# Kernel tuning notes

Hardware: AMD Instinct MI355X
Metric: run time of the kernel (lower is better)

## Reference

```python
import jax, jax.numpy as jnp
import numpy as np

B, H, W = 8, 128, 128
WIDTH, MODES = 32, 12
NL = 6


def _spectral_conv(x, w):
    # x: [B,C,H,W] real; w: [2, Cin, Cout, m, m, 2] (real/imag packed)
    b, c, h, ww = x.shape
    m = w.shape[3]
    xf = jnp.fft.rfft2(x)  # [B,C,H,W//2+1] complex
    w1 = w[0, ..., 0] + 1j * w[0, ..., 1]
    w2 = w[1, ..., 0] + 1j * w[1, ..., 1]
    top = jnp.einsum('bixy,ioxy->boxy', xf[:, :, :m, :m], w1)
    bot = jnp.einsum('bixy,ioxy->boxy', xf[:, :, -m:, :m], w2)
    out = jnp.zeros((b, w.shape[2], h, ww // 2 + 1), dtype=xf.dtype)
    out = out.at[:, :, :m, :m].set(top).at[:, :, -m:, :m].set(bot)
    return jnp.fft.irfft2(out, s=(h, ww))


def _conv1x1(x, wgt, bia):
    # x: [B,C,H,W], wgt: [O,C], bia: [O]
    return jnp.einsum('bchw,oc->bohw', x, wgt) + bia[None, :, None, None]


def _gelu(x):
    return jax.nn.gelu(x, approximate=False)


def setup_inputs() -> dict:
    key = jax.random.key(0)
    ks = jax.random.split(key, 20)
    scale = 1.0 / (WIDTH * WIDTH)
    d = {}
    d['x'] = jax.random.normal(ks[0], (B, H, W, 4), jnp.float32)
    d['fc0_W'] = jax.random.normal(ks[1], (4, WIDTH), jnp.float32) * 0.5
    d['fc0_b'] = jnp.zeros((WIDTH,), jnp.float32)
    d['spec_w'] = scale * jax.random.uniform(ks[2], (NL, 2, WIDTH, WIDTH, MODES, MODES, 2), jnp.float32)
    d['wW'] = jax.random.normal(ks[3], (NL, WIDTH, WIDTH), jnp.float32) * (1.0 / np.sqrt(WIDTH))
    d['wb'] = jnp.zeros((NL, WIDTH), jnp.float32)
    d['bW'] = jax.random.normal(ks[4], (NL, WIDTH, 2), jnp.float32) * 0.7
    d['bb'] = jnp.zeros((NL, WIDTH), jnp.float32)
    d['cW'] = jax.random.normal(ks[5], (NL, WIDTH, 3), jnp.float32) * 0.57
    d['cb'] = jnp.zeros((NL, WIDTH), jnp.float32)
    d['fc1_W'] = jax.random.normal(ks[6], (WIDTH, 256), jnp.float32) * (1.0 / np.sqrt(WIDTH))
    d['fc1_b'] = jnp.zeros((256,), jnp.float32)
    d['fc3_W'] = jax.random.normal(ks[7], (256, 128), jnp.float32) * (1.0 / 16.0)
    d['fc3_b'] = jnp.zeros((128,), jnp.float32)
    d['fc4_W'] = jax.random.normal(ks[8], (128, 128), jnp.float32) * (1.0 / np.sqrt(128.0))
    d['fc4_b'] = jnp.zeros((128,), jnp.float32)
    d['fc5_W'] = jax.random.normal(ks[9], (128, 1), jnp.float32) * (1.0 / np.sqrt(128.0))
    d['fc5_b'] = jnp.zeros((1,), jnp.float32)
    return d


def reference(x, fc0_W, fc0_b, spec_w, wW, wb, bW, bb, cW, cb,
              fc1_W, fc1_b, fc3_W, fc3_b, fc4_W, fc4_b, fc5_W, fc5_b):
    b, h, w, _ = x.shape
    grid_mesh = jnp.transpose(x[:, :, :, 1:4], (0, 3, 1, 2))  # [B,3,H,W]
    y = x @ fc0_W + fc0_b                                     # [B,H,W,width]
    y = jnp.transpose(y, (0, 3, 1, 2))                        # [B,width,H,W]
    gx = jnp.linspace(0.0, 1.0, h, dtype=jnp.float32)
    gy = jnp.linspace(0.0, 1.0, w, dtype=jnp.float32)
    grid = jnp.stack([
        jnp.broadcast_to(gx[:, None], (h, w)),
        jnp.broadcast_to(gy[None, :], (h, w)),
    ], axis=0)                                                # [2,H,W]
    grid = jnp.broadcast_to(grid[None], (b, 2, h, w))
    for l in range(NL):
        y = _gelu(_spectral_conv(y, spec_w[l])
                  + _conv1x1(y, wW[l], wb[l])
                  + _conv1x1(grid, bW[l], bb[l])
                  + _conv1x1(grid_mesh, cW[l], cb[l]))
    y = jnp.transpose(y, (0, 2, 3, 1))                        # [B,H,W,width]
    y = _gelu(y @ fc1_W + fc1_b)
    y = _gelu(y @ fc3_W + fc3_b)
    y = y @ fc4_W + fc4_b
    y = y @ fc5_W + fc5_b
    return y
```

## Files before the change

### kernel.cpp

```cpp
#include <hip/hip_runtime.h>
#include <math.h>


#define NL 6

typedef unsigned short u16;
typedef __attribute__((ext_vector_type(8))) short short8v;
typedef __attribute__((ext_vector_type(8))) unsigned short ushort8v;
typedef __attribute__((ext_vector_type(4))) unsigned short ushort4v;
typedef __attribute__((ext_vector_type(4))) float f32x4;

__device__ __forceinline__ float gelu_f(float x){
  float z  = x*0.70710678118654752f;
  float az = fabsf(z);
  float t  = __builtin_amdgcn_rcpf(fmaf(0.3275911f, az, 1.0f));
  float p  = t*(0.254829592f + t*(-0.284496736f + t*(1.421413741f +
             t*(-1.453152027f + t*1.061405429f))));
  float e  = __expf(-z*z);
  float er = copysignf(fmaf(-p, e, 1.0f), z);
  return 0.5f*x*(1.0f + er);
}
__device__ __forceinline__ u16 f2bf(float x){
  unsigned u = __float_as_uint(x);
  u += 0x7FFF + ((u>>16)&1);
  return (u16)(u>>16);
}
__device__ __forceinline__ float bf2f(u16 h){
  return __uint_as_float(((unsigned)h)<<16);
}
__device__ __forceinline__ void split2(float v, u16 &hh, u16 &ll){
  unsigned u = __float_as_uint(v);
  hh = (u16)(u>>16);
  float lo = v - __uint_as_float(u & 0xFFFF0000u);
  ll = (u16)(__float_as_uint(lo)>>16);
}

__global__ __launch_bounds__(256) void k_fc0f(const float* __restrict__ x,
                      const float* __restrict__ W, const float* __restrict__ b,
                      float* __restrict__ y, float* __restrict__ F1){
  __shared__ float Ws[128];
  __shared__ float bs[32];
  __shared__ float ys2[2][32][132];
  int t = threadIdx.x;
  if (t < 128) Ws[t] = W[t];
  if (t < 32)  bs[t] = b[t];
  __syncthreads();
  int pix = blockIdx.x*256 + t;
  float4 xv = *reinterpret_cast<const float4*>(x + (size_t)pix*4);
  int bb = pix >> 14, hw = pix & 16383;
  int r = t>>7, w = t&127;
  float* yp = y + (size_t)bb*32*16384 + hw;
  #pragma unroll
  for (int c=0;c<32;c++){
    float acc = bs[c] + xv.x*Ws[c] + xv.y*Ws[32+c] + xv.z*Ws[64+c] + xv.w*Ws[96+c];
    yp[(size_t)c*16384] = acc;
    ys2[r][c][w] = acc;
  }
  __syncthreads();
  int c2 = t>>3, wq = t&7;
  float stc[12], sts[12];
  #pragma unroll
  for (int k=0;k<12;k++){ float s,c; sincospif(k*(1.0f/64.0f), &s, &c); stc[k]=c; sts[k]=s; }
  int gr0 = blockIdx.x*2;
  #pragma unroll
  for (int r2=0;r2<2;r2++){
    float cr[12], ci[12], aR[12], aI[12];
    #pragma unroll
    for (int k=0;k<12;k++){
      float s,c; sincospif((float)(k*wq)*0.25f, &s, &c);
      cr[k]=c; ci[k]=s; aR[k]=0.f; aI[k]=0.f;
    }
    const float* rowp = &ys2[r2][c2][wq*16];
    #pragma unroll
    for (int q=0;q<4;q++){
      float4 xq = *reinterpret_cast<const float4*>(rowp + q*4);
      float xa[4]={xq.x,xq.y,xq.z,xq.w};
      #pragma unroll
      for (int e=0;e<4;e++){
        float xw = xa[e];
        #pragma unroll
        for (int k=0;k<12;k++){
          aR[k] += xw*cr[k];
          aI[k] -= xw*ci[k];
          float nc = cr[k]*stc[k] - ci[k]*sts[k];
          ci[k]    = cr[k]*sts[k] + ci[k]*stc[k];
          cr[k] = nc;
        }
      }
    }
    #pragma unroll
    for (int k=0;k<12;k++){
      aR[k] += __shfl_xor(aR[k],1); aR[k] += __shfl_xor(aR[k],2); aR[k] += __shfl_xor(aR[k],4);
      aI[k] += __shfl_xor(aI[k],1); aI[k] += __shfl_xor(aI[k],2); aI[k] += __shfl_xor(aI[k],4);
    }
    if (wq==0){
      int g = gr0 + r2; int b2 = g>>7, h2 = g&127;
      float* dst = F1 + ((size_t)(b2*32+c2)*128 + h2)*24;
      #pragma unroll
      for (int k=0;k<12;k++){ dst[2*k] = aR[k]; dst[2*k+1] = aI[k]; }
    }
  }
}

__global__ __launch_bounds__(256) void k_wtrans(const float* __restrict__ w, float* __restrict__ wT){
  __shared__ float buf[16][32][25];
  int t=threadIdx.x;
  int beta = blockIdx.x;
  int l = beta/48, r = beta%48;
  int hf = r/24; int r2 = r%24;
  int kym = r2>>1; int i0 = (r2&1)*16;
  const float* src = w + (size_t)l*589824 + (size_t)hf*294912 + kym*24;
  float* dst = wT + (size_t)l*589824 + (size_t)hf*294912 + (size_t)kym*24576;
  for (int j=t; j<12288; j+=256){
    int i = j/768, rem = j%768, o = rem/24, kxri = rem%24;
    buf[i][o][kxri] = src[(size_t)(i0+i)*9216 + o*288 + kxri];
  }
  __syncthreads();
  for (int j=t; j<12288; j+=256){
    int kx = j>>10, rem = j&1023, i = rem>>6, orr = rem&63, o = orr>>1, ri = orr&1;
    dst[(size_t)kx*2048 + o*64 + (i0+i)*2 + ri] = buf[i][o][kx*2+ri];
  }
}

__global__ __launch_bounds__(256) void k_wprep(const float* __restrict__ W1, const float* __restrict__ W3,
                       const float* __restrict__ W4,
                       const float* __restrict__ b4, const float* __restrict__ w5,
                       const float* __restrict__ b5,
                       u16* __restrict__ W1h, u16* __restrict__ W1l,
                       u16* __restrict__ W3h, u16* __restrict__ W3l,
                       u16* __restrict__ W4h, u16* __restrict__ W4l,
                       u16* __restrict__ Emh, u16* __restrict__ Eml,
                       u16* __restrict__ E2h, u16* __restrict__ E2l,
                       u16* __restrict__ E3h, u16* __restrict__ E3l,
                       float* __restrict__ c45){
  __shared__ float buf[32][132];
  int t = threadIdx.x, bid = blockIdx.x;
  if (bid < 8){
    int k0 = bid*32;
    for (int i=t;i<4096;i+=256){ int k=i>>7, n=i&127; buf[k][n] = W3[(size_t)(k0+k)*128 + n]; }
    __syncthreads();
    int n = t>>1, kq = t&1;
    #pragma unroll
    for (int kk=0;kk<16;kk++){
      int k = kq*16 + kk;
      float v = buf[k][n];
      u16 hh = f2bf(v);
      W3h[(size_t)bid*4096 + n*32 + k] = hh;
      W3l[(size_t)bid*4096 + n*32 + k] = f2bf(v - bf2f(hh));
    }
  } else if (bid == 8){
    __shared__ float red[256];
    int n = t;
    #pragma unroll
    for (int c=0;c<32;c++){
      float v = W1[(size_t)c*256 + n];
      u16 hh = f2bf(v);
      W1h[n*32 + c] = hh;
      W1l[n*32 + c] = f2bf(v - bf2f(hh));
    }
    red[t] = (t<128)? b4[t]*w5[t] : 0.f;
    __syncthreads();
    for (int s2=128; s2>0; s2>>=1){
      if (t<s2) red[t] += red[t+s2];
      __syncthreads();
    }
    if (t==0) c45[0] = red[0] + b5[0];
  } else if (bid <= 12){
    int k0 = (bid-9)*32;
    for (int i=t;i<4096;i+=256){ int k=i>>7, n=i&127; buf[k][n] = W4[(size_t)(k0+k)*128 + n]; }
    __syncthreads();
    int n = t>>1, kq = t&1;
    #pragma unroll
    for (int kk=0;kk<16;kk++){
      int k = kq*16 + kk;
      float v = buf[k][n];
      u16 hh = f2bf(v);
      W4h[(size_t)(bid-9)*4096 + n*32 + k] = hh;
      W4l[(size_t)(bid-9)*4096 + n*32 + k] = f2bf(v - bf2f(hh));
    }
  } else if (bid == 13){
    for (int i=t;i<4096;i+=256){
      int m=i>>7, w=i&127;
      float v=0.f;
      if (m<24){ float s,c; sincospif((float)((m>>1)*w)*(1.0f/64.0f), &s, &c); v = (m&1)? -s : c; }
      u16 hh, ll; split2(v, hh, ll);
      Emh[i]=hh; Eml[i]=ll;
    }
  } else if (bid == 14){
    for (int i=t;i<12288;i+=256){
      int m=i>>8, k=i&255;
      int kyi = (m<24)? m : m-24;
      int ky  = (kyi<12)? kyi : kyi+104;
      int h   = k&127;
      int mm  = (ky*h)&127;
      float s,c; sincospif((float)mm*(1.0f/64.0f), &s, &c);
      bool sinSlot = k>=128;
      float v;
      if (m<24) v = sinSlot? s : c;
      else      v = sinSlot? c : -s;
      u16 hh, ll; split2(v, hh, ll);
      E2h[i]=hh; E2l[i]=ll;
    }
  } else {
    for (int i=t;i<8192;i+=256){
      int h=i>>6, k=i&63;
      float v=0.f;
      if (k<48){
        int kyi = (k<24)? k : k-24;
        int ky  = (kyi<12)? kyi : kyi+104;
        int mm  = (ky*h)&127;
        float s,c; sincospif((float)mm*(1.0f/64.0f), &s, &c);
        v = ((k<24)? c : s) * (1.0f/16384.0f);
      }
      u16 hh, ll; split2(v, hh, ll);
      E3h[i]=hh; E3l[i]=ll;
    }
  }
}

__global__ __launch_bounds__(256) void k_dfth(const float* __restrict__ F1,
                      const u16* __restrict__ E2h, const u16* __restrict__ E2l,
                      float* __restrict__ F2){
  __shared__ u16 Fth[16*264], Ftl[16*264];
  int t=threadIdx.x;
  int bc = blockIdx.x;
  int b = bc>>5, c = bc&31;
  const float* src = F1 + (size_t)bc*3072;
  for (int i=t;i<3072;i+=256){
    int h = i/24, col = i - h*24;
    int kx = col>>1, ri = col&1;
    u16 hh, ll; split2(src[i], hh, ll);
    int idx = kx*264 + ri*128 + h;
    Fth[idx] = hh; Ftl[idx] = ll;
  }
  __syncthreads();
  int wv = t>>6, lane = t&63, lr = lane&15, lg = lane>>4;
  if (wv < 3){
    f32x4 acc = (f32x4){0.f,0.f,0.f,0.f};
    #pragma unroll
    for (int ks=0; ks<8; ++ks){
      short8v af = *reinterpret_cast<const short8v*>(E2h + (size_t)(wv*16+lr)*256 + ks*32 + lg*8);
      short8v ag = *reinterpret_cast<const short8v*>(E2l + (size_t)(wv*16+lr)*256 + ks*32 + lg*8);
      short8v bf = *reinterpret_cast<const short8v*>(&Fth[lr*264 + ks*32 + lg*8]);
      short8v bg = *reinterpret_cast<const short8v*>(&Ftl[lr*264 + ks*32 + lg*8]);
      acc = __builtin_amdgcn_mfma_f32_16x16x32_bf16(af, bf, acc, 0,0,0);
      acc = __builtin_amdgcn_mfma_f32_16x16x32_bf16(af, bg, acc, 0,0,0);
      acc = __builtin_amdgcn_mfma_f32_16x16x32_bf16(ag, bf, acc, 0,0,0);
    }
    if (lr < 12){
      #pragma unroll
      for (int r=0;r<4;r++){
        int m = wv*16 + 4*lg + r;
        int kyi = (m<24)? m : m-24;
        int ri  = (m<24)? 0 : 1;
        F2[(((size_t)b*24 + kyi)*24 + 2*lr + ri)*32 + c] = acc[r];
      }
    }
  }
}

__global__ __launch_bounds__(576) void k_mixid(const float* __restrict__ F2, const float* __restrict__ wTl,
                      const u16* __restrict__ E3h, const u16* __restrict__ E3l,
                      float* __restrict__ S1){
  __shared__ u16 Bh[32*72], Bl[32*72];
  int t=threadIdx.x;
  int bo = blockIdx.x;
  int b = bo>>5, o = bo&31;
  for (int i=t; i<24*24; i+=576){
    int row = i/24, k = 48 + i - (i/24)*24;
    Bh[row*72 + k] = 0; Bl[row*72 + k] = 0;
  }
  {
    int pair = t>>1, half = t&1;
    int kx = pair%12, kyi = pair/12;
    int hf = kyi<12?0:1, kym = kyi<12?kyi:kyi-12;
    const float* fpr = F2 + (((size_t)b*24 + kyi)*24 + 2*kx)*32 + half*16;
    const float* fpi = fpr + 32;
    const float* wp = wTl + (size_t)(hf*12+kym)*24576 + kx*2048 + o*64 + half*32;
    float gr=0.f, gi=0.f;
    #pragma unroll 8
    for (int i=0;i<16;i++){
      float2 wv = *reinterpret_cast<const float2*>(wp + 2*i);
      float ar = fpr[i], ai = fpi[i];
      gr += ar*wv.x - ai*wv.y;
      gi += ar*wv.y + ai*wv.x;
    }
    gr += __shfl_xor(gr,1);
    gi += __shfl_xor(gi,1);
    if (half==0){
      u16 grh, grl, gih, gil, nih, nil;
      split2(gr, grh, grl);
      split2(gi, gih, gil);
      split2(-gi, nih, nil);
      int r0 = (2*kx)*72, r1 = (2*kx+1)*72;
      Bh[r0 + kyi]      = grh; Bl[r0 + kyi]      = grl;
      Bh[r0 + 24 + kyi] = nih; Bl[r0 + 24 + kyi] = nil;
      Bh[r1 + kyi]      = gih; Bl[r1 + kyi]      = gil;
      Bh[r1 + 24 + kyi] = grh; Bl[r1 + 24 + kyi] = grl;
    }
  }
  __syncthreads();
  int wv = t>>6, lane = t&63, lr = lane&15, lg = lane>>4;
  if (wv < 8){
    f32x4 acc[2];
    acc[0] = (f32x4){0.f,0.f,0.f,0.f};
    acc[1] = (f32x4){0.f,0.f,0.f,0.f};
    #pragma unroll
    for (int ks=0; ks<2; ++ks){
      short8v af = *reinterpret_cast<const short8v*>(E3h + (size_t)(wv*16+lr)*64 + ks*32 + lg*8);
      short8v ag = *reinterpret_cast<const short8v*>(E3l + (size_t)(wv*16+lr)*64 + ks*32 + lg*8);
      #pragma unroll
      for (int nt=0; nt<2; ++nt){
        short8v bf = *reinterpret_cast<const short8v*>(&Bh[(nt*16+lr)*72 + ks*32 + lg*8]);
        short8v bg = *reinterpret_cast<const short8v*>(&Bl[(nt*16+lr)*72 + ks*32 + lg*8]);
        acc[nt] = __builtin_amdgcn_mfma_f32_16x16x32_bf16(af, bf, acc[nt], 0,0,0);
        acc[nt] = __builtin_amdgcn_mfma_f32_16x16x32_bf16(af, bg, acc[nt], 0,0,0);
        acc[nt] = __builtin_amdgcn_mfma_f32_16x16x32_bf16(ag, bf, acc[nt], 0,0,0);
      }
    }
    float* dst = S1 + (size_t)bo*3072;
    #pragma unroll
    for (int nt=0; nt<2; ++nt){
      int n = nt*16 + lr;
      if (n < 24){
        #pragma unroll
        for (int r=0;r<4;r++){
          int h = wv*16 + 4*lg + r;
          dst[h*24 + n] = acc[nt][r];
        }
      }
    }
  }
}

template<int LAST>
__global__ __launch_bounds__(512) void k_combine2(const float* __restrict__ yin, const float* __restrict__ S1,
                         const float* __restrict__ x,
                         const float* __restrict__ wWl, const float* __restrict__ wbl,
                         const float* __restrict__ bWl, const float* __restrict__ bbl,
                         const float* __restrict__ cWl, const float* __restrict__ cbl,
                         const u16* __restrict__ Emh, const u16* __restrict__ Eml,
                         float* __restrict__ yout, float* __restrict__ F1,
                         u16* __restrict__ yb16){
  __shared__ float ysT[128][33];
  __shared__ u16 ybsp[2][32][136];
  int t=threadIdx.x;
  int b = blockIdx.x>>7, h = blockIdx.x&127;
  for (int i=t;i<4096;i+=512){ int c=i>>7, w=i&127;
    ysT[w][c] = yin[(((size_t)(b*32+c))*128+h)*128+w]; }
  __syncthreads();
  int w = t&127;
  int og = __builtin_amdgcn_readfirstlane(t>>7);
  float ct[12], st[12];
  ct[0]=1.f; st[0]=0.f;
  float c1,s1v; sincospif(w*(1.0f/64.0f), &s1v, &c1);
  #pragma unroll
  for (int k=0;k<11;k++){ ct[k+1] = ct[k]*c1 - st[k]*s1v; st[k+1] = ct[k]*s1v + st[k]*c1; }
  float gx = h*(1.0f/127.0f), gy = w*(1.0f/127.0f);
  float4 xm = *reinterpret_cast<const float4*>(x + (((size_t)(b*128+h))*128+w)*4);
  float m1=xm.y, m2=xm.z, m3=xm.w;
  const float* wo  = wWl + og*256;
  const float* s1o = S1 + (size_t)b*98304 + (size_t)og*8*3072 + h*24;
  float accv[8];
  #pragma unroll
  for (int oi=0;oi<8;oi++){
    int o = og*8+oi;
    float bse = wbl[o] + bbl[o] + cbl[o] + gx*bWl[o*2] + gy*bWl[o*2+1]
              + m1*cWl[o*3] + m2*cWl[o*3+1] + m3*cWl[o*3+2];
    const float* sp = s1o + (size_t)oi*3072;
    float spec = sp[0];
    #pragma unroll
    for (int kx=1;kx<12;kx++) spec += 2.0f*(sp[2*kx]*ct[kx] - sp[2*kx+1]*st[kx]);
    accv[oi] = bse + spec;
  }
  #pragma unroll
  for (int c=0;c<32;c++){
    float xc = ysT[w][c];
    #pragma unroll
    for (int oi=0;oi<8;oi++) accv[oi] += wo[oi*32+c]*xc;
  }
  #pragma unroll
  for (int oi=0;oi<8;oi++){
    float g = gelu_f(accv[oi]);
    int o = og*8+oi;
    if constexpr (!LAST){
      u16 hh, ll; split2(g, hh, ll);
      ybsp[0][o][w] = hh;
      ybsp[1][o][w] = ll;
      yout[(((size_t)(b*32+o))*128+h)*128+w] = g;
    } else {
      ybsp[0][o][w] = f2bf(g);
    }
  }
  __syncthreads();
  if constexpr (!LAST){
    int wv = t>>6;
    if (wv < 4){
      int lane = t&63, lr = lane&15, lg = lane>>4;
      int mt = wv&1, oj = wv>>1;
      f32x4 acc = (f32x4){0.f,0.f,0.f,0.f};
      #pragma unroll
      for (int ks=0; ks<4; ++ks){
        short8v ef = *reinterpret_cast<const short8v*>(Emh + (size_t)(mt*16+lr)*128 + ks*32 + lg*8);
        short8v eg = *reinterpret_cast<const short8v*>(Eml + (size_t)(mt*16+lr)*128 + ks*32 + lg*8);
        short8v yf = *reinterpret_cast<const short8v*>(&ybsp[0][oj*16+lr][ks*32+lg*8]);
        short8v yg = *reinterpret_cast<const short8v*>(&ybsp[1][oj*16+lr][ks*32+lg*8]);
        acc = __builtin_amdgcn_mfma_f32_16x16x32_bf16(ef, yf, acc, 0,0,0);
        acc = __builtin_amdgcn_mfma_f32_16x16x32_bf16(ef, yg, acc, 0,0,0);
        acc = __builtin_amdgcn_mfma_f32_16x16x32_bf16(eg, yf, acc, 0,0,0);
      }
      if (mt==0 || lg<2){
        int m = mt*16 + 4*lg;
        int o = oj*16 + lr;
        float4 v; v.x=acc[0]; v.y=acc[1]; v.z=acc[2]; v.w=acc[3];
        *reinterpret_cast<float4*>(&F1[((size_t)(b*32+o)*128 + h)*24 + m]) = v;
      }
    }
  } else {
    int wr = t>>2, hf4 = t&3;
    size_t pix = (size_t)b*16384 + h*128 + wr;
    ushort8v h8;
    #pragma unroll
    for (int q=0;q<8;q++) h8[q] = ybsp[0][hf4*8 + q][wr];
    *reinterpret_cast<ushort8v*>(yb16 + pix*32 + hf4*8) = h8;
  }
}

__global__ __launch_bounds__(256) void k_headm(
    const u16* __restrict__ Yb,
    const u16* __restrict__ W1h, const u16* __restrict__ W1l,
    const float* __restrict__ b1,
    const u16* __restrict__ W3h, const u16* __restrict__ W3l,
    const float* __restrict__ b3,
    const u16* __restrict__ W4h, const u16* __restrict__ W4l,
    const float* __restrict__ c45, const float* __restrict__ w5,
    float* __restrict__ out){
  __shared__ u16 smem[8704];
  __shared__ float b1s[256];
  __shared__ float b3s[128], w5s[128];
  __shared__ float part2[2][64];
  int t = threadIdx.x;
  int wv = t>>6, lane = t&63, lr = lane&15, lg = lane>>4;
  int P0 = blockIdx.x*64;
  b1s[t] = b1[t];
  if (t<128){ b3s[t]=b3[t]; w5s[t]=w5[t]; }
  int wn3 = wv>>1, wp = wv&1;
  short8v yb;
  {
    size_t p = (size_t)P0 + wv*16 + lr;
    yb = *reinterpret_cast<const short8v*>(Yb + p*32 + lg*8);
  }
  f32x4 acc3[4][2];
  #pragma unroll
  for (int i=0;i<4;i++){ acc3[i][0]=(f32x4){0,0,0,0}; acc3[i][1]=(f32x4){0,0,0,0}; }
  __syncthreads();

  auto fc1_into = [&](int kt, u16* dh){
    f32x4 a1[2];
    a1[0]=(f32x4){0,0,0,0}; a1[1]=(f32x4){0,0,0,0};
    #pragma unroll
    for (int i=0;i<2;i++){
      int n1 = kt*32 + i*16 + lr;
      short8v w1f = *reinterpret_cast<const short8v*>(W1h + (size_t)n1*32 + lg*8);
      short8v w1g = *reinterpret_cast<const short8v*>(W1l + (size_t)n1*32 + lg*8);
      a1[i] = __builtin_amdgcn_mfma_f32_16x16x32_bf16(w1f, yb, a1[i], 0,0,0);
      a1[i] = __builtin_amdgcn_mfma_f32_16x16x32_bf16(w1g, yb, a1[i], 0,0,0);
    }
    #pragma unroll
    for (int i=0;i<2;i++){
      int n1b = kt*32 + i*16 + 4*lg;
      int p = wv*16 + lr;
      ushort4v hv;
      #pragma unroll
      for (int r=0;r<4;r++){
        hv[r] = f2bf(gelu_f(a1[i][r] + b1s[n1b+r]));
      }
      *reinterpret_cast<ushort4v*>(&dh[p*40 + i*16+4*lg]) = hv;
    }
  };

  fc1_into(0, smem);
  __syncthreads();
  for (int kt=0; kt<8; ++kt){
    u16* curh = (kt&1)? smem + 2560 : smem;
    if (kt < 7){
      u16* nh = (kt&1)? smem : smem + 2560;
      fc1_into(kt+1, nh);
    }
    short8v ab[2];
    #pragma unroll
    for (int j=0;j<2;j++){
      int pb = wp*32 + j*16 + lr;
      ab[j] = *reinterpret_cast<const short8v*>(&curh[pb*40 + lg*8]);
    }
    #pragma unroll
    for (int i=0;i<4;i++){
      int n3 = wn3*64 + i*16 + lr;
      short8v w3f = *reinterpret_cast<const short8v*>(W3h + (size_t)kt*4096 + n3*32 + lg*8);
      short8v w3g = *reinterpret_cast<const short8v*>(W3l + (size_t)kt*4096 + n3*32 + lg*8);
      #pragma unroll
      for (int j=0;j<2;j++){
        acc3[i][j] = __builtin_amdgcn_mfma_f32_16x16x32_bf16(w3f, ab[j], acc3[i][j], 0,0,0);
        acc3[i][j] = __builtin_amdgcn_mfma_f32_16x16x32_bf16(w3g, ab[j], acc3[i][j], 0,0,0);
      }
    }
    __syncthreads();
  }
  u16* A2 = smem;
  #pragma unroll
  for (int i=0;i<4;i++){
    int n3b = wn3*64 + i*16 + 4*lg;
    #pragma unroll
    for (int j=0;j<2;j++){
      int p = wp*32 + j*16 + lr;
      ushort4v hv;
      #pragma unroll
      for (int r=0;r<4;r++){
        hv[r] = f2bf(gelu_f(acc3[i][j][r] + b3s[n3b+r]));
      }
      *reinterpret_cast<ushort4v*>(&A2[p*136 + n3b]) = hv;
    }
  }
  __syncthreads();
  f32x4 acc4[4][2];
  #pragma unroll
  for (int i=0;i<4;i++){ acc4[i][0]=(f32x4){0,0,0,0}; acc4[i][1]=(f32x4){0,0,0,0}; }
  #pragma unroll
  for (int ks=0; ks<4; ++ks){
    short8v p2[2];
    #pragma unroll
    for (int j=0;j<2;j++){
      int p = wp*32 + j*16 + lr;
      p2[j] = *reinterpret_cast<const short8v*>(&A2[p*136 + ks*32 + lg*8]);
    }
    #pragma unroll
    for (int i2=0;i2<4;i2++){
      int n4 = wn3*64 + i2*16 + lr;
      short8v w4f = *reinterpret_cast<const short8v*>(W4h + (size_t)ks*4096 + n4*32 + lg*8);
      short8v w4g = *reinterpret_cast<const short8v*>(W4l + (size_t)ks*4096 + n4*32 + lg*8);
      #pragma unroll
      for (int j=0;j<2;j++){
        acc4[i2][j] = __builtin_amdgcn_mfma_f32_16x16x32_bf16(w4f, p2[j], acc4[i2][j], 0,0,0);
        acc4[i2][j] = __builtin_amdgcn_mfma_f32_16x16x32_bf16(w4g, p2[j], acc4[i2][j], 0,0,0);
      }
    }
  }
  #pragma unroll
  for (int j=0;j<2;j++){
    float part = 0.f;
    #pragma unroll
    for (int i2=0;i2<4;i2++){
      #pragma unroll
      for (int r=0;r<4;r++){
        int n4 = wn3*64 + i2*16 + 4*lg + r;
        part += acc4[i2][j][r] * w5s[n4];
      }
    }
    part += __shfl_xor(part, 16); part += __shfl_xor(part, 32);
    if (lg==0) part2[wn3][wp*32 + j*16 + lr] = part;
  }
  __syncthreads();
  if (t<64) out[P0 + t] = part2[0][t] + part2[1][t] + c45[0];
}

extern "C" void kernel_launch(void* const* d_in, const int* in_sizes, int n_in,
                              void* d_out, int out_size, void* d_ws, size_t ws_size,
                              hipStream_t stream){
  const float* x     = (const float*)d_in[0];
  const float* fc0_W = (const float*)d_in[1];
  const float* fc0_b = (const float*)d_in[2];
  const float* spec_w= (const float*)d_in[3];
  const float* wW    = (const float*)d_in[4];
  const float* wb    = (const float*)d_in[5];
  const float* bW    = (const float*)d_in[6];
  const float* bb    = (const float*)d_in[7];
  const float* cW    = (const float*)d_in[8];
  const float* cb    = (const float*)d_in[9];
  const float* fc1_W = (const float*)d_in[10];
  const float* fc1_b = (const float*)d_in[11];
  const float* fc3_W = (const float*)d_in[12];
  const float* fc3_b = (const float*)d_in[13];
  const float* fc4_W = (const float*)d_in[14];
  const float* fc4_b = (const float*)d_in[15];
  const float* fc5_W = (const float*)d_in[16];
  const float* fc5_b = (const float*)d_in[17];
  float* out = (float*)d_out;
  float* ws  = (float*)d_ws;

  float* y_a = ws;
  float* y_b = y_a + 4194304;
  float* wT  = y_b + 4194304;
  float* F2  = wT + 3538944;
  float* S1  = F2 + 147456;
  float* F1  = S1 + 786432;
  float* WP  = F1 + 786432;
  u16*   W1h = (u16*)WP;
  u16*   W1l = W1h + 8192;
  u16*   W3h = W1l + 8192;
  u16*   W3l = W3h + 32768;
  u16*   W4h = W3l + 32768;
  u16*   W4l = W4h + 16384;
  u16*   Emh = W4l + 16384;
  u16*   Eml = Emh + 4096;
  u16*   E2h = Eml + 4096;
  u16*   E2l = E2h + 12288;
  u16*   E3h = E2l + 12288;
  u16*   E3l = E3h + 8192;
  float* c45 = (float*)(E3l + 8192);
  u16*   Yb16 = (u16*)y_a;

  k_fc0f<<<512,256,0,stream>>>(x, fc0_W, fc0_b, y_a, F1);
  k_wtrans<<<288,256,0,stream>>>(spec_w, wT);
  k_wprep<<<16,256,0,stream>>>(fc1_W, fc3_W, fc4_W, fc4_b, fc5_W, fc5_b,
                               W1h, W1l, W3h, W3l, W4h, W4l, Emh, Eml,
                               E2h, E2l, E3h, E3l, c45);

  for (int l=0;l<NL;l++){
    float* yin  = (l&1)? y_b : y_a;
    float* yout = (l&1)? y_a : y_b;
    k_dfth<<<256,256,0,stream>>>(F1, E2h, E2l, F2);
    k_mixid<<<256,576,0,stream>>>(F2, wT + (size_t)l*589824, E3h, E3l, S1);
    if (l < NL-1){
      k_combine2<0><<<1024,512,0,stream>>>(yin, S1, x,
                                     wW + (size_t)l*1024, wb + (size_t)l*32,
                                     bW + (size_t)l*64,  bb + (size_t)l*32,
                                     cW + (size_t)l*96,  cb + (size_t)l*32,
                                     Emh, Eml,
                                     yout, F1, nullptr);
    } else {
      k_combine2<1><<<1024,512,0,stream>>>(yin, S1, x,
                                     wW + (size_t)l*1024, wb + (size_t)l*32,
                                     bW + (size_t)l*64,  bb + (size_t)l*32,
                                     cW + (size_t)l*96,  cb + (size_t)l*32,
                                     Emh, Eml,
                                     nullptr, nullptr, Yb16);
    }
  }

  k_headm<<<2048,256,0,stream>>>(Yb16, W1h, W1l, fc1_b, W3h, W3l, fc3_b,
                                 W4h, W4l, c45, fc5_W, out);
}
```

Before: 331.4 us.

## Keep head MLP activations in registers via cross-lane shuffles instead of LDS

Restructures the fused head kernel so each wave owns 16 pixels end to end. MFMA output fragments are repacked into B-operand layout with __shfl rather than being staged through shared memory. This removes the LDS round trips and block-wide barriers between fc1, fc3 and fc4. In exchange each wave now loads the full fc3/fc4 weight tiles for all 128 outputs, adds shuffle instructions, and uses more accumulator registers.

```diff
diff --git a/kernel.cpp b/kernel.cpp
--- a/kernel.cpp
+++ b/kernel.cpp
@@ -33,6 +33,27 @@
   hh = (u16)(u>>16);
   float lo = v - __uint_as_float(u & 0xFFFF0000u);
   ll = (u16)(__float_as_uint(lo)>>16);
+}
+__device__ __forceinline__ short8v repack_pfrag(unsigned qa0, unsigned qa1,
+                                                unsigned qb0, unsigned qb1,
+                                                int lr, int lg){
+  int srcA = lr + 16*((2*lg)&3);
+  int srcB = srcA + 16;
+  unsigned a0 = (unsigned)__shfl((int)qa0, srcA);
+  unsigned a1 = (unsigned)__shfl((int)qa1, srcA);
+  unsigned a2 = (unsigned)__shfl((int)qa0, srcB);
+  unsigned a3 = (unsigned)__shfl((int)qa1, srcB);
+  unsigned b0 = (unsigned)__shfl((int)qb0, srcA);
+  unsigned b1 = (unsigned)__shfl((int)qb1, srcA);
+  unsigned b2 = (unsigned)__shfl((int)qb0, srcB);
+  unsigned b3 = (unsigned)__shfl((int)qb1, srcB);
+  bool hi2 = (lg>=2);
+  union { unsigned u[4]; short8v s; } cv;
+  cv.u[0] = hi2? b0 : a0;
+  cv.u[1] = hi2? b1 : a1;
+  cv.u[2] = hi2? b2 : a2;
+  cv.u[3] = hi2? b3 : a3;
+  return cv.s;
 }
 
 __global__ __launch_bounds__(256) void k_fc0f(const float* __restrict__ x,
@@ -435,27 +456,24 @@
     const u16* __restrict__ W4h, const u16* __restrict__ W4l,
     const float* __restrict__ c45, const float* __restrict__ w5,
     float* __restrict__ out){
-  __shared__ u16 smem[8704];
   __shared__ float b1s[256];
   __shared__ float b3s[128], w5s[128];
-  __shared__ float part2[2][64];
   int t = threadIdx.x;
   int wv = t>>6, lane = t&63, lr = lane&15, lg = lane>>4;
   int P0 = blockIdx.x*64;
   b1s[t] = b1[t];
   if (t<128){ b3s[t]=b3[t]; w5s[t]=w5[t]; }
-  int wn3 = wv>>1, wp = wv&1;
   short8v yb;
   {
     size_t p = (size_t)P0 + wv*16 + lr;
     yb = *reinterpret_cast<const short8v*>(Yb + p*32 + lg*8);
   }
-  f32x4 acc3[4][2];
-  #pragma unroll
-  for (int i=0;i<4;i++){ acc3[i][0]=(f32x4){0,0,0,0}; acc3[i][1]=(f32x4){0,0,0,0}; }
-  __syncthreads();
-
-  auto fc1_into = [&](int kt, u16* dh){
+  f32x4 acc3[8];
+  #pragma unroll
+  for (int i=0;i<8;i++) acc3[i] = (f32x4){0,0,0,0};
+  __syncthreads();
+
+  for (int kt=0; kt<8; ++kt){
     f32x4 a1[2];
     a1[0]=(f32x4){0,0,0,0}; a1[1]=(f32x4){0,0,0,0};
     #pragma unroll
@@ -466,101 +484,64 @@
       a1[i] = __builtin_amdgcn_mfma_f32_16x16x32_bf16(w1f, yb, a1[i], 0,0,0);
       a1[i] = __builtin_amdgcn_mfma_f32_16x16x32_bf16(w1g, yb, a1[i], 0,0,0);
     }
+    unsigned q[2][2];
     #pragma unroll
     for (int i=0;i<2;i++){
       int n1b = kt*32 + i*16 + 4*lg;
-      int p = wv*16 + lr;
-      ushort4v hv;
-      #pragma unroll
-      for (int r=0;r<4;r++){
-        hv[r] = f2bf(gelu_f(a1[i][r] + b1s[n1b+r]));
-      }
-      *reinterpret_cast<ushort4v*>(&dh[p*40 + i*16+4*lg]) = hv;
-    }
-  };
-
-  fc1_into(0, smem);
-  __syncthreads();
-  for (int kt=0; kt<8; ++kt){
-    u16* curh = (kt&1)? smem + 2560 : smem;
-    if (kt < 7){
-      u16* nh = (kt&1)? smem : smem + 2560;
-      fc1_into(kt+1, nh);
-    }
-    short8v ab[2];
-    #pragma unroll
-    for (int j=0;j<2;j++){
-      int pb = wp*32 + j*16 + lr;
-      ab[j] = *reinterpret_cast<const short8v*>(&curh[pb*40 + lg*8]);
-    }
-    #pragma unroll
-    for (int i=0;i<4;i++){
-      int n3 = wn3*64 + i*16 + lr;
+      u16 v0 = f2bf(gelu_f(a1[i][0] + b1s[n1b+0]));
+      u16 v1 = f2bf(gelu_f(a1[i][1] + b1s[n1b+1]));
+      u16 v2 = f2bf(gelu_f(a1[i][2] + b1s[n1b+2]));
+      u16 v3 = f2bf(gelu_f(a1[i][3] + b1s[n1b+3]));
+      q[i][0] = (unsigned)v0 | ((unsigned)v1<<16);
+      q[i][1] = (unsigned)v2 | ((unsigned)v3<<16);
+    }
+    short8v ab = repack_pfrag(q[0][0], q[0][1], q[1][0], q[1][1], lr, lg);
+    #pragma unroll
+    for (int i=0;i<8;i++){
+      int n3 = i*16 + lr;
       short8v w3f = *reinterpret_cast<const short8v*>(W3h + (size_t)kt*4096 + n3*32 + lg*8);
       short8v w3g = *reinterpret_cast<const short8v*>(W3l + (size_t)kt*4096 + n3*32 + lg*8);
-      #pragma unroll
-      for (int j=0;j<2;j++){
-        acc3[i][j] = __builtin_amdgcn_mfma_f32_16x16x32_bf16(w3f, ab[j], acc3[i][j], 0,0,0);
-        acc3[i][j] = __builtin_amdgcn_mfma_f32_16x16x32_bf16(w3g, ab[j], acc3[i][j], 0,0,0);
-      }
-    }
-    __syncthreads();
-  }
-  u16* A2 = smem;
-  #pragma unroll
-  for (int i=0;i<4;i++){
-    int n3b = wn3*64 + i*16 + 4*lg;
-    #pragma unroll
-    for (int j=0;j<2;j++){
-      int p = wp*32 + j*16 + lr;
-      ushort4v hv;
-      #pragma unroll
-      for (int r=0;r<4;r++){
-        hv[r] = f2bf(gelu_f(acc3[i][j][r] + b3s[n3b+r]));
-      }
-      *reinterpret_cast<ushort4v*>(&A2[p*136 + n3b]) = hv;
-    }
-  }
-  __syncthreads();
-  f32x4 acc4[4][2];
-  #pragma unroll
-  for (int i=0;i<4;i++){ acc4[i][0]=(f32x4){0,0,0,0}; acc4[i][1]=(f32x4){0,0,0,0}; }
+      acc3[i] = __builtin_amdgcn_mfma_f32_16x16x32_bf16(w3f, ab, acc3[i], 0,0,0);
+      acc3[i] = __builtin_amdgcn_mfma_f32_16x16x32_bf16(w3g, ab, acc3[i], 0,0,0);
+    }
+  }
+  unsigned q3[8][2];
+  #pragma unroll
+  for (int i=0;i<8;i++){
+    int n3b = i*16 + 4*lg;
+    u16 v0 = f2bf(gelu_f(acc3[i][0] + b3s[n3b+0]));
+    u16 v1 = f2bf(gelu_f(acc3[i][1] + b3s[n3b+1]));
+    u16 v2 = f2bf(gelu_f(acc3[i][2] + b3s[n3b+2]));
+    u16 v3 = f2bf(gelu_f(acc3[i][3] + b3s[n3b+3]));
+    q3[i][0] = (unsigned)v0 | ((unsigned)v1<<16);
+    q3[i][1] = (unsigned)v2 | ((unsigned)v3<<16);
+  }
+  f32x4 acc4[8];
+  #pragma unroll
+  for (int i=0;i<8;i++) acc4[i] = (f32x4){0,0,0,0};
   #pragma unroll
   for (int ks=0; ks<4; ++ks){
-    short8v p2[2];
-    #pragma unroll
-    for (int j=0;j<2;j++){
-      int p = wp*32 + j*16 + lr;
-      p2[j] = *reinterpret_cast<const short8v*>(&A2[p*136 + ks*32 + lg*8]);
-    }
-    #pragma unroll
-    for (int i2=0;i2<4;i2++){
-      int n4 = wn3*64 + i2*16 + lr;
+    short8v pb = repack_pfrag(q3[2*ks][0], q3[2*ks][1], q3[2*ks+1][0], q3[2*ks+1][1], lr, lg);
+    #pragma unroll
+    for (int i2=0;i2<8;i2++){
+      int n4 = i2*16 + lr;
       short8v w4f = *reinterpret_cast<const short8v*>(W4h + (size_t)ks*4096 + n4*32 + lg*8);
       short8v w4g = *reinterpret_cast<const short8v*>(W4l + (size_t)ks*4096 + n4*32 + lg*8);
-      #pragma unroll
-      for (int j=0;j<2;j++){
-        acc4[i2][j] = __builtin_amdgcn_mfma_f32_16x16x32_bf16(w4f, p2[j], acc4[i2][j], 0,0,0);
-        acc4[i2][j] = __builtin_amdgcn_mfma_f32_16x16x32_bf16(w4g, p2[j], acc4[i2][j], 0,0,0);
-      }
-    }
-  }
-  #pragma unroll
-  for (int j=0;j<2;j++){
-    float part = 0.f;
-    #pragma unroll
-    for (int i2=0;i2<4;i2++){
-      #pragma unroll
-      for (int r=0;r<4;r++){
-        int n4 = wn3*64 + i2*16 + 4*lg + r;
-        part += acc4[i2][j][r] * w5s[n4];
-      }
-    }
-    part += __shfl_xor(part, 16); part += __shfl_xor(part, 32);
-    if (lg==0) part2[wn3][wp*32 + j*16 + lr] = part;
-  }
-  __syncthreads();
-  if (t<64) out[P0 + t] = part2[0][t] + part2[1][t] + c45[0];
+      acc4[i2] = __builtin_amdgcn_mfma_f32_16x16x32_bf16(w4f, pb, acc4[i2], 0,0,0);
+      acc4[i2] = __builtin_amdgcn_mfma_f32_16x16x32_bf16(w4g, pb, acc4[i2], 0,0,0);
+    }
+  }
+  float part = 0.f;
+  #pragma unroll
+  for (int i2=0;i2<8;i2++){
+    #pragma unroll
+    for (int r=0;r<4;r++){
+      int n4 = i2*16 + 4*lg + r;
+      part += acc4[i2][r] * w5s[n4];
+    }
+  }
+  part += __shfl_xor(part, 16); part += __shfl_xor(part, 32);
+  if (lg==0) out[P0 + wv*16 + lr] = part + c45[0];
 }
 
 extern "C" void kernel_launch(void* const* d_in, const int* in_sizes, int n_in,
```

New measurement: 369.7 us. 1.12x slower.

## Compute full fc1 activation into shared memory before fc3, removing per-tile barriers

Applied to the files above, without the earlier changes.

The head kernel used to interleave fc1 tile computation with fc3 MFMA accumulation through a double-buffered shared tile, with a block barrier after each of the 8 k-tiles. The new code computes all fc1 outputs (64 pixels x 256) first, packs them in registers, writes them to a larger padded shared buffer, and synchronises once before running fc3 over all k-tiles. This is meant to cut seven block barriers and the serialisation they cause. In exchange it uses more LDS (about 33 KB instead of 17 KB), which may lower occupancy, and holds 32 packed registers per thread.

```diff
diff --git a/kernel.cpp b/kernel.cpp
--- a/kernel.cpp
+++ b/kernel.cpp
@@ -435,7 +435,7 @@
     const u16* __restrict__ W4h, const u16* __restrict__ W4l,
     const float* __restrict__ c45, const float* __restrict__ w5,
     float* __restrict__ out){
-  __shared__ u16 smem[8704];
+  __shared__ u16 Ac[64*264];
   __shared__ float b1s[256];
   __shared__ float b3s[128], w5s[128];
   __shared__ float part2[2][64];
@@ -450,12 +450,11 @@
     size_t p = (size_t)P0 + wv*16 + lr;
     yb = *reinterpret_cast<const short8v*>(Yb + p*32 + lg*8);
   }
-  f32x4 acc3[4][2];
-  #pragma unroll
-  for (int i=0;i<4;i++){ acc3[i][0]=(f32x4){0,0,0,0}; acc3[i][1]=(f32x4){0,0,0,0}; }
-  __syncthreads();
-
-  auto fc1_into = [&](int kt, u16* dh){
+  __syncthreads();
+
+  unsigned q[8][2][2];
+  #pragma unroll
+  for (int kt=0; kt<8; ++kt){
     f32x4 a1[2];
     a1[0]=(f32x4){0,0,0,0}; a1[1]=(f32x4){0,0,0,0};
     #pragma unroll
@@ -469,29 +468,37 @@
     #pragma unroll
     for (int i=0;i<2;i++){
       int n1b = kt*32 + i*16 + 4*lg;
-      int p = wv*16 + lr;
-      ushort4v hv;
-      #pragma unroll
-      for (int r=0;r<4;r++){
-        hv[r] = f2bf(gelu_f(a1[i][r] + b1s[n1b+r]));
-      }
-      *reinterpret_cast<ushort4v*>(&dh[p*40 + i*16+4*lg]) = hv;
-    }
-  };
-
-  fc1_into(0, smem);
-  __syncthreads();
+      u16 v0 = f2bf(gelu_f(a1[i][0] + b1s[n1b+0]));
+      u16 v1 = f2bf(gelu_f(a1[i][1] + b1s[n1b+1]));
+      u16 v2 = f2bf(gelu_f(a1[i][2] + b1s[n1b+2]));
+      u16 v3 = f2bf(gelu_f(a1[i][3] + b1s[n1b+3]));
+      q[kt][i][0] = (unsigned)v0 | ((unsigned)v1<<16);
+      q[kt][i][1] = (unsigned)v2 | ((unsigned)v3<<16);
+    }
+  }
+  {
+    int p = wv*16 + lr;
+    #pragma unroll
+    for (int kt=0; kt<8; ++kt){
+      #pragma unroll
+      for (int i=0;i<2;i++){
+        union { unsigned u[2]; ushort4v s; } cv;
+        cv.u[0] = q[kt][i][0]; cv.u[1] = q[kt][i][1];
+        *reinterpret_cast<ushort4v*>(&Ac[p*264 + kt*32 + i*16 + 4*lg]) = cv.s;
+      }
+    }
+  }
+  __syncthreads();
+  f32x4 acc3[4][2];
+  #pragma unroll
+  for (int i=0;i<4;i++){ acc3[i][0]=(f32x4){0,0,0,0}; acc3[i][1]=(f32x4){0,0,0,0}; }
+  #pragma unroll
   for (int kt=0; kt<8; ++kt){
-    u16* curh = (kt&1)? smem + 2560 : smem;
-    if (kt < 7){
-      u16* nh = (kt&1)? smem : smem + 2560;
-      fc1_into(kt+1, nh);
-    }
     short8v ab[2];
     #pragma unroll
     for (int j=0;j<2;j++){
       int pb = wp*32 + j*16 + lr;
-      ab[j] = *reinterpret_cast<const short8v*>(&curh[pb*40 + lg*8]);
+      ab[j] = *reinterpret_cast<const short8v*>(&Ac[pb*264 + kt*32 + lg*8]);
     }
     #pragma unroll
     for (int i=0;i<4;i++){
@@ -504,9 +511,9 @@
         acc3[i][j] = __builtin_amdgcn_mfma_f32_16x16x32_bf16(w3g, ab[j], acc3[i][j], 0,0,0);
       }
     }
-    __syncthreads();
-  }
-  u16* A2 = smem;
+  }
+  __syncthreads();
+  u16* A2 = Ac;
   #pragma unroll
   for (int i=0;i<4;i++){
     int n3b = wn3*64 + i*16 + 4*lg;
```

Result: no change. 328.2 us (-1.0%).
